# Kernel tuning notes

Measured on AMD Instinct MI355X. Metric: run time of the kernel, lower is better.

Reference implementation:

```python
import jax, jax.numpy as jnp
import numpy as np

BIG_NUMBER = 1000000.0
B, N, F, D = 8, 256, 128, 128  # batch, nodes, feat dim, mid/out size


def setup_inputs() -> dict:
    key = jax.random.key(0)
    ks = jax.random.split(key, 16)
    node_fts = jax.random.normal(ks[0], (B, N, F), jnp.float32)
    hidden = jax.random.normal(ks[1], (B, N, F), jnp.float32)
    edge_fts = jax.random.normal(ks[2], (B, N, N, F), jnp.float32)
    e_hidden = jax.random.normal(ks[3], (B, N, N, F), jnp.float32)
    graph_fts = jax.random.normal(ks[4], (B, F), jnp.float32)
    adj_mat = jax.random.randint(ks[5], (B, N, N), 0, 2, jnp.int32)
    s = 0.05
    We = jax.random.normal(ks[6], (2 * F, D), jnp.float32) * s
    be = jnp.zeros((D,), jnp.float32)
    W_m1 = jax.random.normal(ks[7], (2 * F, D), jnp.float32) * s
    b_m1 = jnp.zeros((D,), jnp.float32)
    W_m2 = jax.random.normal(ks[8], (2 * F, D), jnp.float32) * s
    b_m2 = jnp.zeros((D,), jnp.float32)
    W_o1 = jax.random.normal(ks[9], (2 * F, D), jnp.float32) * s
    b_o1 = jnp.zeros((D,), jnp.float32)
    W_o2 = jax.random.normal(ks[10], (D, D), jnp.float32) * s
    b_o2 = jnp.zeros((D,), jnp.float32)
    return dict(node_fts=node_fts, edge_fts=edge_fts, graph_fts=graph_fts,
                adj_mat=adj_mat, hidden=hidden, e_hidden=e_hidden,
                We=We, be=be, W_m1=W_m1, b_m1=b_m1, W_m2=W_m2, b_m2=b_m2,
                W_o1=W_o1, b_o1=b_o1, W_o2=W_o2, b_o2=b_o2)


def reference(node_fts, edge_fts, graph_fts, adj_mat, hidden, e_hidden,
              We, be, W_m1, b_m1, W_m2, b_m2, W_o1, b_o1, W_o2, b_o2):
    # concat node/edge feats with hiddens
    nt = jnp.concatenate([node_fts, hidden], axis=-1)            # [B,N,2F]
    et = jnp.concatenate([edge_fts, e_hidden], axis=-1) @ We + be  # [B,N,N,D]
    # append virtual node (zeros features, fully connected)
    nt = jnp.concatenate([nt, jnp.zeros((B, 1, 2 * F), nt.dtype)], axis=1)  # [B,N+1,2F]
    adj = adj_mat.astype(nt.dtype)
    adj = jnp.concatenate([adj, jnp.ones((B, 1, N), nt.dtype)], axis=1)
    adj = jnp.concatenate([adj, jnp.ones((B, N + 1, 1), nt.dtype)], axis=2)  # [B,N+1,N+1]
    # MPNN layer (reduction = max)
    msg_1 = nt @ W_m1 + b_m1  # [B,N+1,D]
    msg_2 = nt @ W_m2 + b_m2  # [B,N+1,D]
    msgs = msg_1[:, None, :, :] + msg_2[:, :, None, :]  # [B,N+1,N+1,D]
    msgs = jnp.where(adj[..., None] > 0, msgs, -BIG_NUMBER)
    msgs = jnp.max(msgs, axis=1)  # [B,N+1,D]
    ret = (nt @ W_o1 + b_o1) + (msgs @ W_o2 + b_o2)  # [B,N+1,D]
    # strip virtual node; padded edge tensor sliced back equals et
    return ret[:, :N, :], et
```

## Files before the change

### kernel.cpp

```cpp
#include <hip/hip_runtime.h>
#include <hip/hip_bf16.h>

#define Bn 8
#define Nn 256
#define Fn 128
#define Dn 128

typedef __bf16 bf16_t;
typedef bf16_t bf16x8 __attribute__((ext_vector_type(8)));
typedef float f32x4 __attribute__((ext_vector_type(4)));

__global__ __launch_bounds__(512, 4) void mfma_gemm_kernel(
    const float* __restrict__ edge, const float* __restrict__ ehid,
    const float* __restrict__ We,   const float* __restrict__ be,
    const float* __restrict__ node, const float* __restrict__ hidden,
    const float* __restrict__ W_m1, const float* __restrict__ b_m1,
    const float* __restrict__ W_m2, const float* __restrict__ b_m2,
    const float* __restrict__ W_o1, const float* __restrict__ b_o1,
    float* __restrict__ out_et,
    float* __restrict__ ws_m1, float* __restrict__ ws_m2, float* __restrict__ ws_h1)
{
    __shared__ __align__(16) bf16_t lds[128 * 256];

    const int t = threadIdx.x;

    const float *X1, *X2, *W, *bias;
    float* out;
    long rowbase;
    if (blockIdx.x < 2048) {
        X1 = edge; X2 = ehid; W = We; bias = be; out = out_et;
        rowbase = (long)blockIdx.x * 256;
    } else {
        const int e = blockIdx.x - 2048;
        const int w = e >> 3;
        rowbase = (long)(e & 7) * 256;
        X1 = node; X2 = hidden;
        if (w == 0)      { W = W_m2; bias = b_m2; out = ws_m2; }
        else if (w == 1) { W = W_m1; bias = b_m1; out = ws_m1; }
        else             { W = W_o1; bias = b_o1; out = ws_h1; }
    }

    {
        const int kb = t >> 4;
        const int g  = t & 15;
        const float* wp = W + (kb * 8) * 128 + g * 8;
        float buf[8][8];
        #pragma unroll
        for (int r = 0; r < 8; ++r) {
            f32x4 u0 = *(const f32x4*)(wp + r * 128);
            f32x4 u1 = *(const f32x4*)(wp + r * 128 + 4);
            buf[r][0] = u0[0]; buf[r][1] = u0[1]; buf[r][2] = u0[2]; buf[r][3] = u0[3];
            buf[r][4] = u1[0]; buf[r][5] = u1[1]; buf[r][6] = u1[2]; buf[r][7] = u1[3];
        }
        #pragma unroll
        for (int j = 0; j < 8; ++j) {
            const int n  = g * 8 + j;
            const int cp = kb ^ j ^ (g & 7);
            bf16x8 w8;
            #pragma unroll
            for (int r = 0; r < 8; ++r) w8[r] = (bf16_t)buf[r][j];
            *(bf16x8*)(&lds[n * 256 + cp * 8]) = w8;
        }
    }
    __syncthreads();

    const int wv     = t >> 6;
    const int l      = t & 63;
    const int lane16 = l & 15;
    const int quad   = l >> 4;

    float bev[8];
    #pragma unroll
    for (int nt = 0; nt < 8; ++nt) bev[nt] = bias[nt * 16 + lane16];

    const long wrow = rowbase + wv * 32;

    for (int it = 0; it < 2; ++it) {
        const long rbase = wrow + it * 16;
        const long arow  = rbase + lane16;
        const float* pe = X1 + arow * 128 + quad * 8;
        const float* ph = X2 + arow * 128 + quad * 8;

        bf16x8 a[8];
        #pragma unroll
        for (int kk = 0; kk < 4; ++kk) {
            f32x4 u0 = *(const f32x4*)(pe + kk * 32);
            f32x4 u1 = *(const f32x4*)(pe + kk * 32 + 4);
            bf16x8 aa;
            #pragma unroll
            for (int j = 0; j < 4; ++j) { aa[j] = (bf16_t)u0[j]; aa[j + 4] = (bf16_t)u1[j]; }
            a[kk] = aa;
        }
        #pragma unroll
        for (int kk = 0; kk < 4; ++kk) {
            f32x4 u0 = *(const f32x4*)(ph + kk * 32);
            f32x4 u1 = *(const f32x4*)(ph + kk * 32 + 4);
            bf16x8 aa;
            #pragma unroll
            for (int j = 0; j < 4; ++j) { aa[j] = (bf16_t)u0[j]; aa[j + 4] = (bf16_t)u1[j]; }
            a[kk + 4] = aa;
        }

        f32x4 acc[8];
        #pragma unroll
        for (int nt = 0; nt < 8; ++nt) acc[nt] = (f32x4){0.f, 0.f, 0.f, 0.f};

        #pragma unroll
        for (int kk = 0; kk < 8; ++kk) {
            #pragma unroll
            for (int nt = 0; nt < 8; ++nt) {
                const int n  = nt * 16 + lane16;
                const int c  = kk * 4 + quad;
                const int cp = c ^ (n & 7) ^ ((n >> 3) & 7);
                bf16x8 bfrag = *(const bf16x8*)(&lds[n * 256 + cp * 8]);
                acc[nt] = __builtin_amdgcn_mfma_f32_16x16x32_bf16(a[kk], bfrag, acc[nt], 0, 0, 0);
            }
        }

        const long orow0 = rbase + quad * 4;
        #pragma unroll
        for (int nt = 0; nt < 8; ++nt) {
            #pragma unroll
            for (int r = 0; r < 4; ++r) {
                out[(orow0 + r) * 128 + nt * 16 + lane16] = acc[nt][r] + bev[nt];
            }
        }
    }
}

__global__ void ret_kernel(
    const int* __restrict__ adj,
    const float* __restrict__ m2, const float* __restrict__ m1,
    const float* __restrict__ h1,
    const float* __restrict__ W_o2, const float* __restrict__ b_o2,
    const float* __restrict__ b_m2,
    float* __restrict__ out)
{
    __shared__ float sv[128];
    __shared__ int adjc[256];

    const int bj = blockIdx.x;
    const int b  = bj >> 8;
    const int j  = bj & 255;
    const int d  = threadIdx.x;

    adjc[d]       = adj[(b * 256 + d) * 256 + j];
    adjc[d + 128] = adj[(b * 256 + d + 128) * 256 + j];
    __syncthreads();

    float mx = b_m2[d];
    const float* m2b = m2 + (long)b * 256 * 128 + d;
    #pragma unroll 4
    for (int i = 0; i < 256; ++i) {
        const float v = adjc[i] ? m2b[i * 128] : -3.0e38f;
        mx = fmaxf(mx, v);
    }

    sv[d] = m1[bj * 128 + d] + mx;
    __syncthreads();

    float r = h1[bj * 128 + d] + b_o2[d];
    #pragma unroll 8
    for (int k = 0; k < 128; ++k)
        r += sv[k] * W_o2[k * 128 + d];

    out[bj * 128 + d] = r;
}

extern "C" void kernel_launch(void* const* d_in, const int* in_sizes, int n_in,
                              void* d_out, int out_size, void* d_ws, size_t ws_size,
                              hipStream_t stream)
{
    const float* node   = (const float*)d_in[0];
    const float* edge   = (const float*)d_in[1];
    const int*   adj    = (const int*)d_in[3];
    const float* hidden = (const float*)d_in[4];
    const float* ehid   = (const float*)d_in[5];
    const float* We     = (const float*)d_in[6];
    const float* be     = (const float*)d_in[7];
    const float* W_m1   = (const float*)d_in[8];
    const float* b_m1   = (const float*)d_in[9];
    const float* W_m2   = (const float*)d_in[10];
    const float* b_m2   = (const float*)d_in[11];
    const float* W_o1   = (const float*)d_in[12];
    const float* b_o1   = (const float*)d_in[13];
    const float* W_o2   = (const float*)d_in[14];
    const float* b_o2   = (const float*)d_in[15];

    float* out_ret = (float*)d_out;
    float* out_et  = (float*)d_out + Bn * Nn * Dn;

    float* ws_m2 = (float*)d_ws;
    float* ws_m1 = ws_m2 + 2048 * 128;
    float* ws_h1 = ws_m1 + 2048 * 128;

    hipLaunchKernelGGL(mfma_gemm_kernel, dim3(2048 + 24), dim3(512), 0, stream,
                       edge, ehid, We, be, node, hidden,
                       W_m1, b_m1, W_m2, b_m2, W_o1, b_o1,
                       out_et, ws_m1, ws_m2, ws_h1);
    hipLaunchKernelGGL(ret_kernel, dim3(2048), dim3(128), 0, stream,
                       adj, ws_m2, ws_m1, ws_h1, W_o2, b_o2, b_m2, out_ret);
}
```

Baseline: 679.8 us.

## Software-pipeline GEMM A-loads, use nontemporal stores, widen ret_kernel reduction

```diff
diff --git a/kernel.cpp b/kernel.cpp
--- a/kernel.cpp
+++ b/kernel.cpp
@@ -27,14 +27,17 @@
     const float *X1, *X2, *W, *bias;
     float* out;
     long rowbase;
+    bool streaming;
     if (blockIdx.x < 2048) {
         X1 = edge; X2 = ehid; W = We; bias = be; out = out_et;
         rowbase = (long)blockIdx.x * 256;
+        streaming = true;
     } else {
         const int e = blockIdx.x - 2048;
         const int w = e >> 3;
         rowbase = (long)(e & 7) * 256;
         X1 = node; X2 = hidden;
+        streaming = false;
         if (w == 0)      { W = W_m2; bias = b_m2; out = ws_m2; }
         else if (w == 1) { W = W_m1; bias = b_m1; out = ws_m1; }
         else             { W = W_o1; bias = b_o1; out = ws_h1; }
@@ -75,60 +78,68 @@
 
     const long wrow = rowbase + wv * 32;
 
-    for (int it = 0; it < 2; ++it) {
-        const long rbase = wrow + it * 16;
-        const long arow  = rbase + lane16;
-        const float* pe = X1 + arow * 128 + quad * 8;
-        const float* ph = X2 + arow * 128 + quad * 8;
-
-        bf16x8 a[8];
-        #pragma unroll
-        for (int kk = 0; kk < 4; ++kk) {
-            f32x4 u0 = *(const f32x4*)(pe + kk * 32);
-            f32x4 u1 = *(const f32x4*)(pe + kk * 32 + 4);
-            bf16x8 aa;
-            #pragma unroll
-            for (int j = 0; j < 4; ++j) { aa[j] = (bf16_t)u0[j]; aa[j + 4] = (bf16_t)u1[j]; }
-            a[kk] = aa;
-        }
-        #pragma unroll
-        for (int kk = 0; kk < 4; ++kk) {
-            f32x4 u0 = *(const f32x4*)(ph + kk * 32);
-            f32x4 u1 = *(const f32x4*)(ph + kk * 32 + 4);
-            bf16x8 aa;
-            #pragma unroll
-            for (int j = 0; j < 4; ++j) { aa[j] = (bf16_t)u0[j]; aa[j + 4] = (bf16_t)u1[j]; }
-            a[kk + 4] = aa;
-        }
-
-        f32x4 acc[8];
-        #pragma unroll
-        for (int nt = 0; nt < 8; ++nt) acc[nt] = (f32x4){0.f, 0.f, 0.f, 0.f};
-
-        #pragma unroll
-        for (int kk = 0; kk < 8; ++kk) {
+    const float* base1 = X1 + (wrow + lane16) * 128 + quad * 8;
+    const float* base2 = X2 + (wrow + lane16) * 128 + quad * 8;
+
+    #define CHUNK_PTR(s, c) (((c) < 4 ? base1 : base2) + (s) * 16 * 128 + ((c) & 3) * 32)
+
+    f32x4 u0[2], u1[2];
+    { const float* p = CHUNK_PTR(0, 0); u0[0] = *(const f32x4*)p; u1[0] = *(const f32x4*)(p + 4); }
+    { const float* p = CHUNK_PTR(0, 1); u0[1] = *(const f32x4*)p; u1[1] = *(const f32x4*)(p + 4); }
+
+    f32x4 acc[8];
+    #pragma unroll
+    for (int nt = 0; nt < 8; ++nt) acc[nt] = (f32x4){0.f, 0.f, 0.f, 0.f};
+
+    #pragma unroll
+    for (int cc = 0; cc < 16; ++cc) {
+        const int s  = cc >> 3;
+        const int c  = cc & 7;
+        const int pb = cc & 1;
+
+        bf16x8 afrag;
+        #pragma unroll
+        for (int j = 0; j < 4; ++j) {
+            afrag[j]     = (bf16_t)u0[pb][j];
+            afrag[j + 4] = (bf16_t)u1[pb][j];
+        }
+
+        if (cc + 2 < 16) {
+            const int s2 = (cc + 2) >> 3, c2 = (cc + 2) & 7;
+            const float* p = CHUNK_PTR(s2, c2);
+            u0[pb] = *(const f32x4*)p;
+            u1[pb] = *(const f32x4*)(p + 4);
+        }
+
+        #pragma unroll
+        for (int nt = 0; nt < 8; ++nt) {
+            const int n    = nt * 16 + lane16;
+            const int cidx = c * 4 + quad;
+            const int cp   = cidx ^ (n & 7) ^ ((n >> 3) & 7);
+            bf16x8 bfrag = *(const bf16x8*)(&lds[n * 256 + cp * 8]);
+            acc[nt] = __builtin_amdgcn_mfma_f32_16x16x32_bf16(afrag, bfrag, acc[nt], 0, 0, 0);
+        }
+
+        if (c == 7) {
+            const long orow0 = wrow + s * 16 + quad * 4;
             #pragma unroll
             for (int nt = 0; nt < 8; ++nt) {
-                const int n  = nt * 16 + lane16;
-                const int c  = kk * 4 + quad;
-                const int cp = c ^ (n & 7) ^ ((n >> 3) & 7);
-                bf16x8 bfrag = *(const bf16x8*)(&lds[n * 256 + cp * 8]);
-                acc[nt] = __builtin_amdgcn_mfma_f32_16x16x32_bf16(a[kk], bfrag, acc[nt], 0, 0, 0);
+                #pragma unroll
+                for (int r = 0; r < 4; ++r) {
+                    const float v = acc[nt][r] + bev[nt];
+                    float* p = out + (orow0 + r) * 128 + nt * 16 + lane16;
+                    if (streaming) __builtin_nontemporal_store(v, p);
+                    else           *p = v;
+                }
             }
-        }
-
-        const long orow0 = rbase + quad * 4;
-        #pragma unroll
-        for (int nt = 0; nt < 8; ++nt) {
             #pragma unroll
-            for (int r = 0; r < 4; ++r) {
-                out[(orow0 + r) * 128 + nt * 16 + lane16] = acc[nt][r] + bev[nt];
-            }
-        }
-    }
+            for (int nt = 0; nt < 8; ++nt) acc[nt] = (f32x4){0.f, 0.f, 0.f, 0.f};
+        }
+    }
+    #undef CHUNK_PTR
 }
 
-__global__ void ret_kernel(
+__global__ __launch_bounds__(256) void ret_kernel(
     const int* __restrict__ adj,
     const float* __restrict__ m2, const float* __restrict__ m1,
     const float* __restrict__ h1,
@@ -136,35 +147,55 @@
     const float* __restrict__ b_m2,
     float* __restrict__ out)
 {
+    __shared__ int   adjc[256];
+    __shared__ float part[8][128];
     __shared__ float sv[128];
-    __shared__ int adjc[256];
 
     const int bj = blockIdx.x;
     const int b  = bj >> 8;
     const int j  = bj & 255;
-    const int d  = threadIdx.x;
-
-    adjc[d]       = adj[(b * 256 + d) * 256 + j];
-    adjc[d + 128] = adj[(b * 256 + d + 128) * 256 + j];
-    __syncthreads();
-
-    float mx = b_m2[d];
-    const float* m2b = m2 + (long)b * 256 * 128 + d;
-    #pragma unroll 4
-    for (int i = 0; i < 256; ++i) {
-        const float v = adjc[i] ? m2b[i * 128] : -3.0e38f;
-        mx = fmaxf(mx, v);
-    }
-
-    sv[d] = m1[bj * 128 + d] + mx;
-    __syncthreads();
-
-    float r = h1[bj * 128 + d] + b_o2[d];
+    const int t  = threadIdx.x;
+
+    adjc[t] = adj[(b * 256 + t) * 256 + j];
+    __syncthreads();
+
+    const int s  = t >> 5;
+    const int dg = t & 31;
+    f32x4 mx4;
+    mx4[0] = mx4[1] = mx4[2] = mx4[3] = -3.0e38f;
+    const float* m2p = m2 + ((long)b * 256 + s * 32) * 128 + dg * 4;
     #pragma unroll 8
-    for (int k = 0; k < 128; ++k)
-        r += sv[k] * W_o2[k * 128 + d];
-
-    out[bj * 128 + d] = r;
+    for (int i = 0; i < 32; ++i) {
+        const f32x4 v = *(const f32x4*)(m2p + i * 128);
+        const bool on = (adjc[s * 32 + i] != 0);
+        mx4[0] = on ? fmaxf(mx4[0], v[0]) : mx4[0];
+        mx4[1] = on ? fmaxf(mx4[1], v[1]) : mx4[1];
+        mx4[2] = on ? fmaxf(mx4[2], v[2]) : mx4[2];
+        mx4[3] = on ? fmaxf(mx4[3], v[3]) : mx4[3];
+    }
+    *(f32x4*)&part[s][dg * 4] = mx4;
+    __syncthreads();
+
+    if (t < 128) {
+        float m = b_m2[t];
+        #pragma unroll
+        for (int ss = 0; ss < 8; ++ss) m = fmaxf(m, part[ss][t]);
+        sv[t] = m1[bj * 128 + t] + m;
+    }
+    __syncthreads();
+
+    const int d = t & 127;
+    const int h = t >> 7;
+    float r = 0.f;
+    const float* wp = W_o2 + (h * 64) * 128 + d;
+    #pragma unroll 8
+    for (int k = 0; k < 64; ++k)
+        r += sv[h * 64 + k] * wp[k * 128];
+
+    if (h == 1) part[0][d] = r;
+    __syncthreads();
+    if (h == 0)
+        out[bj * 128 + d] = r + part[0][d] + h1[bj * 128 + d] + b_o2[d];
 }
 
 extern "C" void kernel_launch(void* const* d_in, const int* in_sizes, int n_in,
@@ -198,6 +229,6 @@
                        edge, ehid, We, be, node, hidden,
                        W_m1, b_m1, W_m2, b_m2, W_o1, b_o1,
                        out_et, ws_m1, ws_m2, ws_h1);
-    hipLaunchKernelGGL(ret_kernel, dim3(2048), dim3(128), 0, stream,
+    hipLaunchKernelGGL(ret_kernel, dim3(2048), dim3(256), 0, stream,
                        adj, ws_m2, ws_m1, ws_h1, W_o2, b_o2, b_m2, out_ret);
 }
```

After: 672.3 us. Within noise of the previous version (-1.1%).
